# Kernel tuning notes

Hardware: AMD Instinct MI355X
Metric: run time of the kernel (lower is better)

## Reference

```python
import jax, jax.numpy as jnp
import numpy as np

D_MODEL = 512
DEPTH = 2
D_STATE = 16
D_CONV = 4
EXPAND = 2
D_INNER = EXPAND * D_MODEL
DT_RANK = (D_MODEL + 15) // 16  # ceil(d_model/16) = 32
B_SZ = 8
SEQ = 2048


def setup_inputs() -> dict:
    key = jax.random.key(0)
    ks = jax.random.split(key, 8)
    s = 0.02
    A0 = jnp.log(jnp.broadcast_to(jnp.arange(1, D_STATE + 1, dtype=jnp.float32),
                                  (DEPTH, D_INNER, D_STATE)))
    return {
        "x": jax.random.normal(ks[0], (B_SZ, SEQ, D_MODEL), jnp.float32),
        "ln_w": jnp.ones((DEPTH, D_MODEL), jnp.float32),
        "ln_b": jnp.zeros((DEPTH, D_MODEL), jnp.float32),
        "in_proj_w": jax.random.normal(ks[1], (DEPTH, 2 * D_INNER, D_MODEL), jnp.float32) * s,
        "conv_w": jax.random.normal(ks[2], (DEPTH, D_INNER, 1, D_CONV), jnp.float32) * s,
        "conv_b": jnp.zeros((DEPTH, D_INNER), jnp.float32),
        "x_proj_w": jax.random.normal(ks[3], (DEPTH, DT_RANK + 2 * D_STATE, D_INNER), jnp.float32) * s,
        "dt_proj_w": jax.random.normal(ks[4], (DEPTH, D_INNER, DT_RANK), jnp.float32) * s,
        "dt_proj_b": jax.random.uniform(ks[5], (DEPTH, D_INNER), jnp.float32, -4.0, -2.0),
        "A_log": A0,
        "D_param": jnp.ones((DEPTH, D_INNER), jnp.float32),
        "out_proj_w": jax.random.normal(ks[6], (DEPTH, D_MODEL, D_INNER), jnp.float32) * s,
    }


def _layer_norm(x, w, b):
    mu = x.mean(-1, keepdims=True)
    var = ((x - mu) ** 2).mean(-1, keepdims=True)
    return (x - mu) * jax.lax.rsqrt(var + 1e-5) * w + b


def _mamba_block(x, in_w, cw, cb, xp_w, dtw, dtb, A_log, Dp, ow):
    B = x.shape[0]
    # input projection -> x branch and gate z
    xz = jnp.einsum('bld,ed->ble', x, in_w)          # [B,L,2*d_inner]
    xi, z = jnp.split(xz, 2, axis=-1)
    # depthwise causal conv1d over time
    xc = jnp.transpose(xi, (0, 2, 1))                 # [B,d_inner,L]
    xc = jax.lax.conv_general_dilated(
        xc, cw, (1,), [(D_CONV - 1, 0)],
        dimension_numbers=('NCH', 'OIH', 'NCH'),
        feature_group_count=D_INNER)
    xc = xc + cb[None, :, None]
    xi = jax.nn.silu(jnp.transpose(xc, (0, 2, 1)))    # [B,L,d_inner]
    # input-dependent dt, B, C
    dbc = jnp.einsum('ble,fe->blf', xi, xp_w)         # [B,L,dt_rank+2*d_state]
    dt = dbc[..., :DT_RANK]
    Bm = dbc[..., DT_RANK:DT_RANK + D_STATE]
    Cm = dbc[..., DT_RANK + D_STATE:]
    delta = jax.nn.softplus(jnp.einsum('blr,er->ble', dt, dtw) + dtb)  # [B,L,d_inner]
    A = -jnp.exp(A_log)                               # [d_inner,d_state]

    def step(h, ins):
        d_t, B_t, C_t, u_t = ins                      # [B,E],[B,N],[B,N],[B,E]
        dA = jnp.exp(d_t[..., None] * A)              # [B,E,N]
        h = dA * h + (d_t * u_t)[..., None] * B_t[:, None, :]
        y = jnp.einsum('ben,bn->be', h, C_t)
        return h, y

    h0 = jnp.zeros((B, D_INNER, D_STATE), x.dtype)
    ins = (jnp.transpose(delta, (1, 0, 2)),
           jnp.transpose(Bm, (1, 0, 2)),
           jnp.transpose(Cm, (1, 0, 2)),
           jnp.transpose(xi, (1, 0, 2)))
    _, ys = jax.lax.scan(step, h0, ins)               # ys: [L,B,d_inner]
    y = jnp.transpose(ys, (1, 0, 2)) + xi * Dp        # skip term D*u
    y = y * jax.nn.silu(z)                            # gate
    return jnp.einsum('ble,de->bld', y, ow)           # out projection


def reference(x, ln_w, ln_b, in_proj_w, conv_w, conv_b, x_proj_w,
              dt_proj_w, dt_proj_b, A_log, D_param, out_proj_w):
    for i in range(DEPTH):
        x = x + _mamba_block(_layer_norm(x, ln_w[i], ln_b[i]),
                             in_proj_w[i], conv_w[i], conv_b[i], x_proj_w[i],
                             dt_proj_w[i], dt_proj_b[i], A_log[i], D_param[i],
                             out_proj_w[i])
    return x
```

## Files before the change

kernel.cpp:

```cpp
#include <hip/hip_runtime.h>
#include <hip/hip_bf16.h>
#include <math.h>

#define B_SZ   8
#define SEQ    2048
#define DMODEL 512
#define DEPTH  2
#define DSTATE 16
#define DCONV  4
#define DINNER 1024
#define DTRANK 32
#define ROWS   (B_SZ * SEQ)
#define DBCW   (DTRANK + 2 * DSTATE)

typedef unsigned short u16;
typedef float f32x4 __attribute__((ext_vector_type(4)));
typedef short bf16x8 __attribute__((ext_vector_type(8)));

__device__ __forceinline__ float silu_f(float v) {
    return v * __builtin_amdgcn_rcpf(1.f + __expf(-v));
}
__device__ __forceinline__ float softplus_f(float s) {
    return (s > 20.f) ? s : __logf(1.f + __expf(s));
}
__device__ __forceinline__ u16 f2b(float v) {
    __hip_bfloat16 h = __float2bfloat16(v);
    return *(u16*)&h;
}
__device__ __forceinline__ float b2f(u16 v) {
    __hip_bfloat16 h;
    *(u16*)&h = v;
    return __bfloat162float(h);
}
__device__ __forceinline__ float sum16(float x) {
    x += __int_as_float(__builtin_amdgcn_update_dpp(0, __float_as_int(x), 0x121, 0xf, 0xf, true));
    x += __int_as_float(__builtin_amdgcn_update_dpp(0, __float_as_int(x), 0x122, 0xf, 0xf, true));
    x += __int_as_float(__builtin_amdgcn_update_dpp(0, __float_as_int(x), 0x124, 0xf, 0xf, true));
    x += __int_as_float(__builtin_amdgcn_update_dpp(0, __float_as_int(x), 0x128, 0xf, 0xf, true));
    return x;
}

__device__ __forceinline__ void load_lds16(const void* g, void* l) {
    __builtin_amdgcn_global_load_lds(
        (const __attribute__((address_space(1))) unsigned int*)g,
        (__attribute__((address_space(3))) unsigned int*)l, 16, 0, 0);
}

#define N_INW  (2 * DINNER * DMODEL)
#define N_OUTW (DMODEL * DINNER)
#define N_XW   (DBCW * DINNER)
__global__ __launch_bounds__(256) void conv_weights(const float* __restrict__ iw,
                                                    const float* __restrict__ ow,
                                                    const float* __restrict__ xw,
                                                    u16* __restrict__ inwbf,
                                                    u16* __restrict__ outwbf,
                                                    u16* __restrict__ xwbf) {
    int i = blockIdx.x * 256 + threadIdx.x;
    if (i < N_INW) inwbf[i] = f2b(iw[i]);
    else if (i < N_INW + N_OUTW) outwbf[i - N_INW] = f2b(ow[i - N_INW]);
    else if (i < N_INW + N_OUTW + N_XW) xwbf[i - N_INW - N_OUTW] = f2b(xw[i - N_INW - N_OUTW]);
}

__global__ __launch_bounds__(256) void ln_kernel(const float* __restrict__ x,
                                                 const float* __restrict__ w,
                                                 const float* __restrict__ b,
                                                 u16* __restrict__ out) {
    int r = blockIdx.x;
    int tid = threadIdx.x;
    const float* xr = x + (size_t)r * DMODEL;
    float2 v = *(const float2*)(xr + tid * 2);
    float s = v.x + v.y;
    float s2 = v.x * v.x + v.y * v.y;
    #pragma unroll
    for (int off = 1; off < 64; off <<= 1) {
        s  += __shfl_xor(s, off);
        s2 += __shfl_xor(s2, off);
    }
    __shared__ float ws[4], ws2[4];
    int wid = tid >> 6, lane = tid & 63;
    if (lane == 0) { ws[wid] = s; ws2[wid] = s2; }
    __syncthreads();
    float ts = ws[0] + ws[1] + ws[2] + ws[3];
    float ts2 = ws2[0] + ws2[1] + ws2[2] + ws2[3];
    float mean = ts * (1.f / DMODEL);
    float var = ts2 * (1.f / DMODEL) - mean * mean;
    float inv = rsqrtf(var + 1e-5f);
    out[(size_t)r * DMODEL + tid * 2]     = f2b((v.x - mean) * inv * w[tid * 2] + b[tid * 2]);
    out[(size_t)r * DMODEL + tid * 2 + 1] = f2b((v.y - mean) * inv * w[tid * 2 + 1] + b[tid * 2 + 1]);
}

__global__ __launch_bounds__(256) void gemm_in(const u16* __restrict__ A,
                                               const u16* __restrict__ W,
                                               u16* __restrict__ xi_re,
                                               u16* __restrict__ sz_re) {
    __shared__ u16 As[128 * 32];
    __shared__ u16 Bs[128 * 32];
    const int K = DMODEL;
    int tid = threadIdx.x;
    int wave = tid >> 6, lane = tid & 63;
    int wm = (wave >> 1) * 64, wn = (wave & 1) * 64;
    int m0 = blockIdx.y * 128, n0 = blockIdx.x * 128;
    int srow = lane >> 2, sseg = lane & 3;
    const u16* Ag = A + (size_t)(m0 + wave * 32 + srow) * K + sseg * 8;
    const u16* Wg = W + (size_t)(n0 + wave * 32 + srow) * K + sseg * 8;
    u16* Asw = As + wave * 32 * 32;
    u16* Bsw = Bs + wave * 32 * 32;

    f32x4 acc[4][4] = {};
    int col = lane & 15, quad = lane >> 4;

    for (int k0 = 0; k0 < K; k0 += 32) {
        __syncthreads();
        load_lds16(Ag + k0, Asw);
        load_lds16(Ag + k0 + (size_t)16 * K, Asw + 16 * 32);
        load_lds16(Wg + k0, Bsw);
        load_lds16(Wg + k0 + (size_t)16 * K, Bsw + 16 * 32);
        __syncthreads();
        bf16x8 af[4], bfr[4];
        #pragma unroll
        for (int i = 0; i < 4; ++i) {
            af[i]  = *(const bf16x8*)(As + (wm + i * 16 + col) * 32 + quad * 8);
            bfr[i] = *(const bf16x8*)(Bs + (wn + i * 16 + col) * 32 + quad * 8);
        }
        #pragma unroll
        for (int i = 0; i < 4; ++i)
            #pragma unroll
            for (int j = 0; j < 4; ++j)
                acc[i][j] = __builtin_amdgcn_mfma_f32_16x16x32_bf16(af[i], bfr[j], acc[i][j], 0, 0, 0);
    }
    bool is_z = (n0 >= DINNER);
    u16* dst = is_z ? sz_re : xi_re;
    int nb = n0 & (DINNER - 1);
    #pragma unroll
    for (int i = 0; i < 4; ++i) {
        int gm_base = m0 + wm + i * 16 + quad * 4;
        #pragma unroll
        for (int j = 0; j < 4; ++j) {
            int gn = nb + wn + j * 16 + col;
            #pragma unroll
            for (int r = 0; r < 4; ++r) {
                float v = acc[i][j][r];
                if (is_z) v = silu_f(v);
                dst[(size_t)(gm_base + r) * DINNER + gn] = f2b(v);
            }
        }
    }
}

__global__ __launch_bounds__(256) void gemm_out(const u16* __restrict__ A,
                                                const u16* __restrict__ W,
                                                const float* __restrict__ res,
                                                float* __restrict__ C) {
    __shared__ u16 As[128 * 32];
    __shared__ u16 Bs[128 * 32];
    const int K = DINNER, N = DMODEL;
    int tid = threadIdx.x;
    int wave = tid >> 6, lane = tid & 63;
    int wm = (wave >> 1) * 64, wn = (wave & 1) * 64;
    int m0 = blockIdx.y * 128, n0 = blockIdx.x * 128;
    int srow = lane >> 2, sseg = lane & 3;
    const u16* Ag = A + (size_t)(m0 + wave * 32 + srow) * K + sseg * 8;
    const u16* Wg = W + (size_t)(n0 + wave * 32 + srow) * K + sseg * 8;
    u16* Asw = As + wave * 32 * 32;
    u16* Bsw = Bs + wave * 32 * 32;

    f32x4 acc[4][4] = {};
    int col = lane & 15, quad = lane >> 4;

    for (int k0 = 0; k0 < K; k0 += 32) {
        __syncthreads();
        load_lds16(Ag + k0, Asw);
        load_lds16(Ag + k0 + (size_t)16 * K, Asw + 16 * 32);
        load_lds16(Wg + k0, Bsw);
        load_lds16(Wg + k0 + (size_t)16 * K, Bsw + 16 * 32);
        __syncthreads();
        bf16x8 af[4], bfr[4];
        #pragma unroll
        for (int i = 0; i < 4; ++i) {
            af[i]  = *(const bf16x8*)(As + (wm + i * 16 + col) * 32 + quad * 8);
            bfr[i] = *(const bf16x8*)(Bs + (wn + i * 16 + col) * 32 + quad * 8);
        }
        #pragma unroll
        for (int i = 0; i < 4; ++i)
            #pragma unroll
            for (int j = 0; j < 4; ++j)
                acc[i][j] = __builtin_amdgcn_mfma_f32_16x16x32_bf16(af[i], bfr[j], acc[i][j], 0, 0, 0);
    }
    #pragma unroll
    for (int i = 0; i < 4; ++i) {
        int gm_base = m0 + wm + i * 16 + quad * 4;
        #pragma unroll
        for (int j = 0; j < 4; ++j) {
            int gn = n0 + wn + j * 16 + col;
            #pragma unroll
            for (int r = 0; r < 4; ++r) {
                size_t off = (size_t)(gm_base + r) * N + gn;
                C[off] = acc[i][j][r] + res[off];
            }
        }
    }
}

__global__ __launch_bounds__(256) void gemm_xp_bf16(const u16* __restrict__ A,
                                                    const u16* __restrict__ W,
                                                    float* __restrict__ C) {
    __shared__ u16 As[128 * 32];
    __shared__ u16 Bs[64 * 32];
    int tid = threadIdx.x;
    int wave = tid >> 6, lane = tid & 63;
    int m0 = blockIdx.x * 128;
    int wm = wave * 32;
    int srow = lane >> 2, sseg = lane & 3;
    const u16* Ag = A + (size_t)(m0 + wm + srow) * DINNER + sseg * 8;
    const u16* Wg = W + (size_t)(wave * 16 + srow) * DINNER + sseg * 8;
    u16* Asw = As + wave * 32 * 32;
    u16* Bsw = Bs + wave * 16 * 32;

    f32x4 acc[2][4] = {};
    int col = lane & 15, quad = lane >> 4;

    for (int k0 = 0; k0 < DINNER; k0 += 32) {
        __syncthreads();
        load_lds16(Ag + k0, Asw);
        load_lds16(Ag + k0 + (size_t)16 * DINNER, Asw + 16 * 32);
        load_lds16(Wg + k0, Bsw);
        __syncthreads();
        bf16x8 af[2], bfr[4];
        #pragma unroll
        for (int i = 0; i < 2; ++i)
            af[i] = *(const bf16x8*)(As + (wm + i * 16 + col) * 32 + quad * 8);
        #pragma unroll
        for (int j = 0; j < 4; ++j)
            bfr[j] = *(const bf16x8*)(Bs + (j * 16 + col) * 32 + quad * 8);
        #pragma unroll
        for (int i = 0; i < 2; ++i)
            #pragma unroll
            for (int j = 0; j < 4; ++j)
                acc[i][j] = __builtin_amdgcn_mfma_f32_16x16x32_bf16(af[i], bfr[j], acc[i][j], 0, 0, 0);
    }
    #pragma unroll
    for (int i = 0; i < 2; ++i) {
        int gm_base = m0 + wm + i * 16 + quad * 4;
        #pragma unroll
        for (int j = 0; j < 4; ++j) {
            int gn = j * 16 + col;
            #pragma unroll
            for (int r = 0; r < 4; ++r)
                C[(size_t)(gm_base + r) * DBCW + gn] = acc[i][j][r];
        }
    }
}

__global__ __launch_bounds__(256) void u_t_kernel(const u16* __restrict__ xi_re,
                                                  const u16* __restrict__ sz_re,
                                                  const float* __restrict__ cw,
                                                  const float* __restrict__ cb,
                                                  u16* __restrict__ ut,
                                                  u16* __restrict__ u_re,
                                                  u16* __restrict__ szt) {
    __shared__ float xt[67][65];
    __shared__ u16 uo[64][70];
    __shared__ u16 szo[64][70];
    int tid = threadIdx.x;
    int t0 = blockIdx.x * 64, e0 = blockIdx.y * 64, b = blockIdx.z;
    int er = tid & 63, rr = tid >> 6;
    for (int it = 0; it < 17; ++it) {
        int row = it * 4 + rr;
        if (row < 67) {
            int t = t0 + row - 3;
            xt[row][er] = (t >= 0) ? b2f(xi_re[((size_t)b * SEQ + t) * DINNER + e0 + er]) : 0.f;
        }
    }
    #pragma unroll
    for (int it = 0; it < 16; ++it) {
        int row = it * 4 + rr;
        szo[er][row] = sz_re[((size_t)b * SEQ + t0 + row) * DINNER + e0 + er];
    }
    __syncthreads();
    {
        int e = tid & 63, tg = tid >> 6;
        float4 w4 = *(const float4*)(cw + (e0 + e) * 4);
        float cbe = cb[e0 + e];
        int tl0 = tg * 16;
        float x3 = xt[tl0][e], x2 = xt[tl0 + 1][e], x1 = xt[tl0 + 2][e];
        #pragma unroll
        for (int i = 0; i < 16; ++i) {
            float x0 = xt[tl0 + i + 3][e];
            float u = silu_f(cbe + w4.x * x3 + w4.y * x2 + w4.z * x1 + w4.w * x0);
            x3 = x2; x2 = x1; x1 = x0;
            u16 ub = f2b(u);
            uo[e][tl0 + i] = ub;
            u_re[((size_t)b * SEQ + t0 + tl0 + i) * DINNER + e0 + e] = ub;
        }
    }
    __syncthreads();
    {
        int tl = tid & 63, eg = tid >> 6;
        #pragma unroll
        for (int i = 0; i < 16; ++i) {
            int ee = eg * 16 + i;
            ut[((size_t)b * DINNER + e0 + ee) * SEQ + t0 + tl] = uo[ee][tl];
            szt[((size_t)b * DINNER + e0 + ee) * SEQ + t0 + tl] = szo[ee][tl];
        }
    }
}

__global__ __launch_bounds__(256) void delta_bct_kernel(const float* __restrict__ dbc,
                                                        const float* __restrict__ dtw,
                                                        const float* __restrict__ dtb,
                                                        u16* __restrict__ dlt,
                                                        u16* __restrict__ Bt,
                                                        u16* __restrict__ Ct) {
    __shared__ float wl[64 * 32];
    __shared__ float bl[64];
    int tid = threadIdx.x;
    int e0 = blockIdx.x * 64, t0 = blockIdx.y * 256, b = blockIdx.z;
    for (int i = tid; i < 64 * 32; i += 256) wl[i] = dtw[(size_t)e0 * DTRANK + i];
    if (tid < 64) bl[tid] = dtb[e0 + tid];
    float dreg[32];
    const float* dp = dbc + (size_t)(b * SEQ + t0 + tid) * DBCW;
    #pragma unroll
    for (int k = 0; k < 32; k += 4) {
        float4 v = *(const float4*)(dp + k);
        dreg[k] = v.x; dreg[k + 1] = v.y; dreg[k + 2] = v.z; dreg[k + 3] = v.w;
    }
    __syncthreads();
    for (int ep = 0; ep < 64; ++ep) {
        float s = bl[ep];
        #pragma unroll
        for (int k = 0; k < 32; ++k) s += dreg[k] * wl[ep * 32 + k];
        dlt[((size_t)b * DINNER + e0 + ep) * SEQ + t0 + tid] = f2b(softplus_f(s));
    }
    if (blockIdx.x == 0) {
        int t = t0 + tid;
        const float* dp2 = dbc + (size_t)(b * SEQ + t) * DBCW + DTRANK;
        #pragma unroll
        for (int nn = 0; nn < DSTATE; ++nn) {
            Bt[((size_t)b * DSTATE + nn) * SEQ + t] = f2b(dp2[nn]);
            Ct[((size_t)b * DSTATE + nn) * SEQ + t] = f2b(dp2[DSTATE + nn]);
        }
    }
}

#define SCHUNK 16

struct ChunkBuf {
    bf16x8 u0, u1, d0, d1, b0, b1, c0, c1;
    u16 uo_r, szo_r;
};

__global__ __launch_bounds__(256, 2) void scan_fused(u16* __restrict__ y_re,
                                                     const u16* __restrict__ ut,
                                                     const u16* __restrict__ dlt,
                                                     const u16* __restrict__ Bt,
                                                     const u16* __restrict__ Ct,
                                                     const u16* __restrict__ szt,
                                                     const float* __restrict__ Alog,
                                                     const float* __restrict__ Dp) {
    int tid = threadIdx.x;
    int pair = tid >> 4, n = tid & 15;
    int blk = blockIdx.x;
    int b = blk >> 6;
    int e = ((blk & 63) << 4) + pair;
    float a2 = -__expf(Alog[e * DSTATE + n]) * 1.44269504f;
    float dpe = Dp[e];
    const u16* urow  = ut  + ((size_t)b * DINNER + e) * SEQ;
    const u16* dlrow = dlt + ((size_t)b * DINNER + e) * SEQ;
    const u16* szrow = szt + ((size_t)b * DINNER + e) * SEQ;
    const u16* Brow  = Bt + ((size_t)b * DSTATE + n) * SEQ;
    const u16* Crow  = Ct + ((size_t)b * DSTATE + n) * SEQ;
    u16* ystore = y_re + ((size_t)b * SEQ + n) * DINNER + e;

    float msk[16];
    #pragma unroll
    for (int j = 0; j < 16; ++j) msk[j] = (n == j) ? 1.f : 0.f;

    float h = 0.f;
    ChunkBuf bufA, bufB, bufC, bufD;

    auto load = [&](int c, ChunkBuf& R) {
        R.u0 = *(const bf16x8*)(urow + c * SCHUNK);
        R.u1 = *(const bf16x8*)(urow + c * SCHUNK + 8);
        R.d0 = *(const bf16x8*)(dlrow + c * SCHUNK);
        R.d1 = *(const bf16x8*)(dlrow + c * SCHUNK + 8);
        R.b0 = *(const bf16x8*)(Brow + c * SCHUNK);
        R.b1 = *(const bf16x8*)(Brow + c * SCHUNK + 8);
        R.c0 = *(const bf16x8*)(Crow + c * SCHUNK);
        R.c1 = *(const bf16x8*)(Crow + c * SCHUNK + 8);
        R.uo_r  = urow[c * SCHUNK + n];
        R.szo_r = szrow[c * SCHUNK + n];
    };
    auto proc = [&](int c, const ChunkBuf& R) {
        float keep = 0.f;
        #pragma unroll
        for (int j = 0; j < SCHUNK; ++j) {
            float uf = b2f((u16)((j < 8) ? R.u0[j] : R.u1[j - 8]));
            float dl = b2f((u16)((j < 8) ? R.d0[j] : R.d1[j - 8]));
            float dA = __builtin_amdgcn_exp2f(dl * a2);
            h = dA * h + (dl * uf) * b2f((u16)((j < 8) ? R.b0[j] : R.b1[j - 8]));
            float yp = sum16(h * b2f((u16)((j < 8) ? R.c0[j] : R.c1[j - 8])));
            keep += yp * msk[j];
        }
        ystore[(size_t)c * SCHUNK * DINNER] =
            f2b((keep + b2f(R.uo_r) * dpe) * b2f(R.szo_r));
    };

    const int nc = SEQ / SCHUNK;
    load(0, bufA);
    load(1, bufB);
    load(2, bufC);
    __builtin_amdgcn_sched_barrier(0);
    for (int c = 0; c < nc; c += 4) {
        int c3 = c + 3, c4 = c + 4, c5 = c + 5, c6 = c + 6;
        c4 = (c4 < nc) ? c4 : nc - 1;
        c5 = (c5 < nc) ? c5 : nc - 1;
        c6 = (c6 < nc) ? c6 : nc - 1;
        load(c3, bufD);  __builtin_amdgcn_sched_barrier(0);  proc(c,     bufA);
        load(c4, bufA);  __builtin_amdgcn_sched_barrier(0);  proc(c + 1, bufB);
        load(c5, bufB);  __builtin_amdgcn_sched_barrier(0);  proc(c + 2, bufC);
        load(c6, bufC);  __builtin_amdgcn_sched_barrier(0);  proc(c + 3, bufD);
    }
}

extern "C" void kernel_launch(void* const* d_in, const int* in_sizes, int n_in,
                              void* d_out, int out_size, void* d_ws, size_t ws_size,
                              hipStream_t stream) {
    const float* x_in   = (const float*)d_in[0];
    const float* ln_w   = (const float*)d_in[1];
    const float* ln_b   = (const float*)d_in[2];
    const float* inw    = (const float*)d_in[3];
    const float* convw  = (const float*)d_in[4];
    const float* convb  = (const float*)d_in[5];
    const float* xpw    = (const float*)d_in[6];
    const float* dtw    = (const float*)d_in[7];
    const float* dtb    = (const float*)d_in[8];
    const float* Alog   = (const float*)d_in[9];
    const float* Dp     = (const float*)d_in[10];
    const float* outw   = (const float*)d_in[11];
    float* out = (float*)d_out;

    char* p = (char*)d_ws;
    u16* xi_re = (u16*)p;               p += (size_t)ROWS * DINNER * 2;
    u16* sz_re = (u16*)p;               p += (size_t)ROWS * DINNER * 2;
    u16* y_re  = (u16*)p;               p += (size_t)ROWS * DINNER * 2;
    float* dbc = (float*)p;             p += (size_t)ROWS * DBCW * 4;
    u16* dlt   = (u16*)p;               p += (size_t)B_SZ * DINNER * SEQ * 2;
    u16* u_re  = dlt;
    u16* Bt    = (u16*)p;               p += (size_t)B_SZ * DSTATE * SEQ * 2;
    u16* xwbf  = Bt;
    u16* Ct    = (u16*)p;               p += (size_t)B_SZ * DSTATE * SEQ * 2;
    u16* ut    = (u16*)p;               p += (size_t)B_SZ * DINNER * SEQ * 2;
    u16* xnbf  = ut;
    u16* szt   = (u16*)p;               p += (size_t)B_SZ * DINNER * SEQ * 2;
    u16* inwbf = (u16*)p;               p += (size_t)N_INW * 2;
    u16* outwbf = (u16*)p;              p += (size_t)N_OUTW * 2;

    const dim3 blk256(256);
    const int n_conv = N_INW + N_OUTW + N_XW;

    for (int i = 0; i < DEPTH; ++i) {
        const float* x_cur = (i == 0) ? x_in : out;
        const float* lw  = ln_w  + (size_t)i * DMODEL;
        const float* lb  = ln_b  + (size_t)i * DMODEL;
        const float* iw  = inw   + (size_t)i * 2 * DINNER * DMODEL;
        const float* cw  = convw + (size_t)i * DINNER * DCONV;
        const float* cb  = convb + (size_t)i * DINNER;
        const float* xw  = xpw   + (size_t)i * DBCW * DINNER;
        const float* dw  = dtw   + (size_t)i * DINNER * DTRANK;
        const float* db  = dtb   + (size_t)i * DINNER;
        const float* Al  = Alog  + (size_t)i * DINNER * DSTATE;
        const float* Dpp = Dp    + (size_t)i * DINNER;
        const float* ow  = outw  + (size_t)i * DMODEL * DINNER;

        conv_weights<<<(n_conv + 255) / 256, blk256, 0, stream>>>(
            iw, ow, xw, inwbf, outwbf, xwbf);
        ln_kernel<<<ROWS, blk256, 0, stream>>>(x_cur, lw, lb, xnbf);
        gemm_in<<<dim3(2 * DINNER / 128, ROWS / 128), blk256, 0, stream>>>(
            xnbf, inwbf, xi_re, sz_re);
        u_t_kernel<<<dim3(SEQ / 64, DINNER / 64, B_SZ), blk256, 0, stream>>>(
            xi_re, sz_re, cw, cb, ut, u_re, szt);
        gemm_xp_bf16<<<ROWS / 128, blk256, 0, stream>>>(u_re, xwbf, dbc);
        delta_bct_kernel<<<dim3(DINNER / 64, SEQ / 256, B_SZ), blk256, 0, stream>>>(
            dbc, dw, db, dlt, Bt, Ct);
        scan_fused<<<(B_SZ * DINNER) / 16, blk256, 0, stream>>>(
            y_re, ut, dlt, Bt, Ct, szt, Al, Dpp);
        gemm_out<<<dim3(DMODEL / 128, ROWS / 128), blk256, 0, stream>>>(
            y_re, outwbf, x_cur, out);
    }
}
```

Before: 860.9 us.

## Write in-projection output transposed via LDS and simplify conv kernel

The in-projection GEMM epilogue now stages its tile through shared memory and writes x and silu(z) directly in a channel-major [B,E,L] layout with 16-byte vector stores. The conv kernel then reads each channel's time series contiguously, and the separate transpose of silu(z) plus one full round trip of z through memory are gone. This trades an extra LDS pass and two barriers in the GEMM epilogue for less global traffic and fewer scattered 2-byte stores. The row-major u_re output is still produced through an LDS transpose.

```diff
diff --git a/kernel.cpp b/kernel.cpp
--- a/kernel.cpp
+++ b/kernel.cpp
@@ -91,10 +91,11 @@
 
 __global__ __launch_bounds__(256) void gemm_in(const u16* __restrict__ A,
                                                const u16* __restrict__ W,
-                                               u16* __restrict__ xi_re,
-                                               u16* __restrict__ sz_re) {
+                                               u16* __restrict__ xt,
+                                               u16* __restrict__ szt) {
     __shared__ u16 As[128 * 32];
     __shared__ u16 Bs[128 * 32];
+    __shared__ u16 ts[64 * 136];
     const int K = DMODEL;
     int tid = threadIdx.x;
     int wave = tid >> 6, lane = tid & 63;
@@ -128,22 +129,41 @@
             for (int j = 0; j < 4; ++j)
                 acc[i][j] = __builtin_amdgcn_mfma_f32_16x16x32_bf16(af[i], bfr[j], acc[i][j], 0, 0, 0);
     }
+
     bool is_z = (n0 >= DINNER);
-    u16* dst = is_z ? sz_re : xi_re;
+    u16* dstT = is_z ? szt : xt;
     int nb = n0 & (DINNER - 1);
-    #pragma unroll
-    for (int i = 0; i < 4; ++i) {
-        int gm_base = m0 + wm + i * 16 + quad * 4;
-        #pragma unroll
-        for (int j = 0; j < 4; ++j) {
-            int gn = nb + wn + j * 16 + col;
+    int bb = m0 >> 11;
+    int t0 = m0 & (SEQ - 1);
+
+    for (int hp = 0; hp < 2; ++hp) {
+        __syncthreads();
+        if ((wave & 1) == hp) {
             #pragma unroll
-            for (int r = 0; r < 4; ++r) {
-                float v = acc[i][j][r];
-                if (is_z) v = silu_f(v);
-                dst[(size_t)(gm_base + r) * DINNER + gn] = f2b(v);
-            }
-        }
+            for (int i = 0; i < 4; ++i)
+                #pragma unroll
+                for (int j = 0; j < 4; ++j)
+                    #pragma unroll
+                    for (int r = 0; r < 4; ++r) {
+                        int row = wm + i * 16 + quad * 4 + r;
+                        int cl  = j * 16 + col;
+                        float v = acc[i][j][r];
+                        if (is_z) v = silu_f(v);
+                        ts[cl * 136 + row] = f2b(v);
+                    }
+        }
+        __syncthreads();
+        int cl = tid >> 2, tp = tid & 3;
+        const u16* src = ts + cl * 136 + tp * 32;
+        bf16x8 o0 = *(const bf16x8*)(src);
+        bf16x8 o1 = *(const bf16x8*)(src + 8);
+        bf16x8 o2 = *(const bf16x8*)(src + 16);
+        bf16x8 o3 = *(const bf16x8*)(src + 24);
+        u16* d = dstT + ((size_t)bb * DINNER + nb + hp * 64 + cl) * SEQ + t0 + tp * 32;
+        *(bf16x8*)(d)      = o0;
+        *(bf16x8*)(d + 8)  = o1;
+        *(bf16x8*)(d + 16) = o2;
+        *(bf16x8*)(d + 24) = o3;
     }
 }
 
@@ -251,56 +271,46 @@
     }
 }
 
-__global__ __launch_bounds__(256) void u_t_kernel(const u16* __restrict__ xi_re,
-                                                  const u16* __restrict__ sz_re,
+__global__ __launch_bounds__(256) void u_t_kernel(const u16* __restrict__ xt,
                                                   const float* __restrict__ cw,
                                                   const float* __restrict__ cb,
                                                   u16* __restrict__ ut,
-                                                  u16* __restrict__ u_re,
-                                                  u16* __restrict__ szt) {
-    __shared__ float xt[67][65];
+                                                  u16* __restrict__ u_re) {
     __shared__ u16 uo[64][70];
-    __shared__ u16 szo[64][70];
     int tid = threadIdx.x;
     int t0 = blockIdx.x * 64, e0 = blockIdx.y * 64, b = blockIdx.z;
-    int er = tid & 63, rr = tid >> 6;
-    for (int it = 0; it < 17; ++it) {
-        int row = it * 4 + rr;
-        if (row < 67) {
-            int t = t0 + row - 3;
-            xt[row][er] = (t >= 0) ? b2f(xi_re[((size_t)b * SEQ + t) * DINNER + e0 + er]) : 0.f;
-        }
-    }
+    int el = tid & 63, tg = tid >> 6;
+    int e = e0 + el;
+    int tbase = t0 + tg * 16;
+    const u16* row = xt + ((size_t)b * DINNER + e) * SEQ;
+    bf16x8 s0, s1, s2;
+    if (tbase >= 8) s0 = *(const bf16x8*)(row + tbase - 8);
+    else            s0 = (bf16x8){0, 0, 0, 0, 0, 0, 0, 0};
+    s1 = *(const bf16x8*)(row + tbase);
+    s2 = *(const bf16x8*)(row + tbase + 8);
+    float4 w4 = *(const float4*)(cw + e * 4);
+    float cbe = cb[e];
+    float x3 = b2f((u16)s0[5]), x2 = b2f((u16)s0[6]), x1 = b2f((u16)s0[7]);
+    bf16x8 o0, o1;
     #pragma unroll
-    for (int it = 0; it < 16; ++it) {
-        int row = it * 4 + rr;
-        szo[er][row] = sz_re[((size_t)b * SEQ + t0 + row) * DINNER + e0 + er];
-    }
-    __syncthreads();
-    {
-        int e = tid & 63, tg = tid >> 6;
-        float4 w4 = *(const float4*)(cw + (e0 + e) * 4);
-        float cbe = cb[e0 + e];
-        int tl0 = tg * 16;
-        float x3 = xt[tl0][e], x2 = xt[tl0 + 1][e], x1 = xt[tl0 + 2][e];
-        #pragma unroll
-        for (int i = 0; i < 16; ++i) {
-            float x0 = xt[tl0 + i + 3][e];
-            float u = silu_f(cbe + w4.x * x3 + w4.y * x2 + w4.z * x1 + w4.w * x0);
-            x3 = x2; x2 = x1; x1 = x0;
-            u16 ub = f2b(u);
-            uo[e][tl0 + i] = ub;
-            u_re[((size_t)b * SEQ + t0 + tl0 + i) * DINNER + e0 + e] = ub;
-        }
-    }
+    for (int i = 0; i < 16; ++i) {
+        float x0 = b2f((u16)((i < 8) ? s1[i] : s2[i - 8]));
+        float u = silu_f(cbe + w4.x * x3 + w4.y * x2 + w4.z * x1 + w4.w * x0);
+        x3 = x2; x2 = x1; x1 = x0;
+        u16 ub = f2b(u);
+        if (i < 8) o0[i] = (short)ub; else o1[i - 8] = (short)ub;
+        uo[el][tg * 16 + i] = ub;
+    }
+    u16* ud = ut + ((size_t)b * DINNER + e) * SEQ + tbase;
+    *(bf16x8*)(ud)     = o0;
+    *(bf16x8*)(ud + 8) = o1;
     __syncthreads();
     {
         int tl = tid & 63, eg = tid >> 6;
         #pragma unroll
         for (int i = 0; i < 16; ++i) {
             int ee = eg * 16 + i;
-            ut[((size_t)b * DINNER + e0 + ee) * SEQ + t0 + tl] = uo[ee][tl];
-            szt[((size_t)b * DINNER + e0 + ee) * SEQ + t0 + tl] = szo[ee][tl];
+            u_re[((size_t)b * SEQ + t0 + tl) * DINNER + e0 + ee] = uo[ee][tl];
         }
     }
 }
@@ -440,8 +450,8 @@
     float* out = (float*)d_out;
 
     char* p = (char*)d_ws;
-    u16* xi_re = (u16*)p;               p += (size_t)ROWS * DINNER * 2;
-    u16* sz_re = (u16*)p;               p += (size_t)ROWS * DINNER * 2;
+    u16* xt    = (u16*)p;               p += (size_t)ROWS * DINNER * 2;
+    u16* szt   = (u16*)p;               p += (size_t)ROWS * DINNER * 2;
     u16* y_re  = (u16*)p;               p += (size_t)ROWS * DINNER * 2;
     float* dbc = (float*)p;             p += (size_t)ROWS * DBCW * 4;
     u16* dlt   = (u16*)p;               p += (size_t)B_SZ * DINNER * SEQ * 2;
@@ -451,7 +461,8 @@
     u16* Ct    = (u16*)p;               p += (size_t)B_SZ * DSTATE * SEQ * 2;
     u16* ut    = (u16*)p;               p += (size_t)B_SZ * DINNER * SEQ * 2;
     u16* xnbf  = ut;
-    u16* szt   = (u16*)p;               p += (size_t)B_SZ * DINNER * SEQ * 2;
+    u16* spare = (u16*)p;               p += (size_t)B_SZ * DINNER * SEQ * 2;
+    (void)spare;
     u16* inwbf = (u16*)p;               p += (size_t)N_INW * 2;
     u16* outwbf = (u16*)p;              p += (size_t)N_OUTW * 2;
 
@@ -476,9 +487,9 @@
             iw, ow, xw, inwbf, outwbf, xwbf);
         ln_kernel<<<ROWS, blk256, 0, stream>>>(x_cur, lw, lb, xnbf);
         gemm_in<<<dim3(2 * DINNER / 128, ROWS / 128), blk256, 0, stream>>>(
-            xnbf, inwbf, xi_re, sz_re);
+            xnbf, inwbf, xt, szt);
         u_t_kernel<<<dim3(SEQ / 64, DINNER / 64, B_SZ), blk256, 0, stream>>>(
-            xi_re, sz_re, cw, cb, ut, u_re, szt);
+            xt, cw, cb, ut, u_re);
         gemm_xp_bf16<<<ROWS / 128, blk256, 0, stream>>>(u_re, xwbf, dbc);
         delta_bct_kernel<<<dim3(DINNER / 64, SEQ / 256, B_SZ), blk256, 0, stream>>>(
             dbc, dw, db, dlt, Bt, Ct);
```

New measurement: 920.1 us. 6.9% more time.
